# Kernel optimization log

Measured on AMD Instinct MI355X. Metric: run time of the kernel, lower is better.

The kernel has to match this reference:

```python
import jax, jax.numpy as jnp
import numpy as np
import math

B, S, L, D, H, F = 4, 1024, 4, 256, 8, 1024
NUM_LETTERS = 22
VOCAB = NUM_LETTERS + 3
HD = D // H
DISSONANCE = 0.5


def setup_inputs() -> dict:
    key = jax.random.key(0)
    ks = iter(jax.random.split(key, 64))
    r = lambda shape, s=0.05: jax.random.normal(next(ks), shape, dtype=jnp.float32) * s
    inp = {
        'input_roots': jax.random.randint(next(ks), (B, S, 3), 0, VOCAB),
        'gematria': jax.random.uniform(next(ks), (B, S), dtype=jnp.float32),
        'letter_embed': r((VOCAB, D), 0.02),
        'root_proj_w': r((3 * D, D)), 'root_proj_b': jnp.zeros((D,)),
        'root_ln_g': jnp.ones((D,)), 'root_ln_b': jnp.zeros((D,)),
        'input_proj_w': r((2 * D, D)), 'input_proj_b': jnp.zeros((D,)),
        'input_ln_g': jnp.ones((D,)), 'input_ln_b': jnp.zeros((D,)),
        'qw': r((L, D, D)), 'qb': jnp.zeros((L, D)),
        'kw': r((L, D, D)), 'kb': jnp.zeros((L, D)),
        'vw': r((L, D, D)), 'vb': jnp.zeros((L, D)),
        'ow': r((L, D, D)), 'ob': jnp.zeros((L, D)),
        'dist_scale': r((L, H), 0.1), 'diss_sens': jnp.full((L, H), 0.5),
        'ff1w': r((L, D, F)), 'ff1b': jnp.zeros((L, F)),
        'ff2w': r((L, F, D)), 'ff2b': jnp.zeros((L, D)),
        'ln1g': jnp.ones((L, D)), 'ln1b': jnp.zeros((L, D)),
        'ln2g': jnp.ones((L, D)), 'ln2b': jnp.zeros((L, D)),
        'out_ln_g': jnp.ones((D,)), 'out_ln_b': jnp.zeros((D,)),
        'h1w': r((D, NUM_LETTERS)), 'h1b': jnp.zeros((NUM_LETTERS,)),
        'h2w': r((D, NUM_LETTERS)), 'h2b': jnp.zeros((NUM_LETTERS,)),
        'h3w': r((D, NUM_LETTERS)), 'h3b': jnp.zeros((NUM_LETTERS,)),
    }
    return inp


def _ln(x, g, b):
    m = jnp.mean(x, -1, keepdims=True)
    v = jnp.mean(jnp.square(x - m), -1, keepdims=True)
    return (x - m) * jax.lax.rsqrt(v + 1e-5) * g + b


def _rtl_pos(s, d):
    # flipped sinusoidal PE: token j gets original position s-1-j
    pos = (s - 1 - jnp.arange(s, dtype=jnp.float32))[:, None]
    div = jnp.exp(jnp.arange(0, d, 2, dtype=jnp.float32) * (-(math.log(10000.0) / d)))
    pe = jnp.zeros((s, d))
    pe = pe.at[:, 0::2].set(jnp.sin(pos * div))
    pe = pe.at[:, 1::2].set(jnp.cos(pos * div))
    return pe


def _forward(input_roots, gematria, letter_embed, root_proj_w, root_proj_b,
             root_ln_g, root_ln_b, input_proj_w, input_proj_b, input_ln_g, input_ln_b,
             qw, qb, kw, kb, vw, vb, ow, ob, dist_scale, diss_sens,
             ff1w, ff1b, ff2w, ff2b, ln1g, ln1b, ln2g, ln2b,
             out_ln_g, out_ln_b, h1w, h1b, h2w, h2b, h3w, h3b):
    b, s, _ = input_roots.shape
    # root encoder
    letters = letter_embed[input_roots]                      # (b,s,3,D)
    root_emb = _ln(letters.reshape(b, s, 3 * D) @ root_proj_w + root_proj_b, root_ln_g, root_ln_b)
    # gematria sinusoidal
    angles = (gematria[..., None] * 500.0) * jnp.exp(
        jnp.arange(0, D, 2, dtype=jnp.float32) * (-(math.log(10000.0) / D)))
    gem_emb = jnp.concatenate([jnp.sin(angles), jnp.cos(angles)], axis=-1)  # (b,s,D)
    x = jnp.concatenate([root_emb, gem_emb], axis=-1) @ input_proj_w + input_proj_b
    x = _ln(x + _rtl_pos(s, D)[None], input_ln_g, input_ln_b)
    # distance matrix |i-j| shared across layers
    pos = jnp.arange(s, dtype=jnp.float32)
    dist = jnp.abs(pos[None, :] - pos[:, None])              # (s,s)
    scale = 1.0 / math.sqrt(HD)
    for i in range(L):
        normed = _ln(x, ln1g[i], ln1b[i])
        Q = (normed @ qw[i] + qb[i]).reshape(b, s, H, HD)
        K = (normed @ kw[i] + kb[i]).reshape(b, s, H, HD)
        V = (normed @ vw[i] + vb[i]).reshape(b, s, H, HD)
        scores = jnp.einsum('bqhd,bkhd->bhqk', Q, K) * scale
        penalty = dist_scale[i] * (1.0 - DISSONANCE * diss_sens[i])  # (H,)
        bias = -jnp.abs(penalty)[:, None, None] * dist[None]         # (H,s,s)
        attn = jax.nn.softmax(scores + bias[None], axis=-1)
        out = jnp.einsum('bhqk,bkhd->bqhd', attn, V).reshape(b, s, D)
        x = x + (out @ ow[i] + ob[i])
        h = _ln(x, ln2g[i], ln2b[i])
        x = x + (jax.nn.gelu(h @ ff1w[i] + ff1b[i], approximate=False) @ ff2w[i] + ff2b[i])
    x = _ln(x, out_ln_g, out_ln_b)
    return (x @ h1w + h1b, x @ h2w + h2b, x @ h3w + h3b)


def reference(input_roots, gematria, letter_embed, root_proj_w, root_proj_b,
              root_ln_g, root_ln_b, input_proj_w, input_proj_b, input_ln_g, input_ln_b,
              qw, qb, kw, kb, vw, vb, ow, ob, dist_scale, diss_sens,
              ff1w, ff1b, ff2w, ff2b, ln1g, ln1b, ln2g, ln2b,
              out_ln_g, out_ln_b, h1w, h1b, h2w, h2b, h3w, h3b):
    return _forward(input_roots, gematria, letter_embed, root_proj_w, root_proj_b,
                    root_ln_g, root_ln_b, input_proj_w, input_proj_b, input_ln_g, input_ln_b,
                    qw, qb, kw, kb, vw, vb, ow, ob, dist_scale, diss_sens,
                    ff1w, ff1b, ff2w, ff2b, ln1g, ln1b, ln2g, ln2b,
                    out_ln_g, out_ln_b, h1w, h1b, h2w, h2b, h3w, h3b)
```

## Files before the change

### kernel.cpp

```cpp
#include <hip/hip_runtime.h>
#include <hip/hip_bf16.h>
#include <math.h>

#define NTOK   4096
#define SEQ    1024
#define DMODEL 256
#define NHEAD  8
#define FDIM   1024
#define NLAYER 4

typedef __attribute__((ext_vector_type(8))) short short8v;
typedef __attribute__((ext_vector_type(4))) float f32x4;

#define LDS3(p) ((__attribute__((address_space(3))) unsigned int*)(p))
#define GAS1(p) ((const __attribute__((address_space(1))) unsigned int*)(p))

__device__ __forceinline__ void gl_lds16(const void* g, void* l) {
    __builtin_amdgcn_global_load_lds(GAS1(g), LDS3(l), 16, 0, 0);
}
__device__ __forceinline__ short f2bf(float v) {
    __hip_bfloat16 h = __float2bfloat16(v);
    return __builtin_bit_cast(short, h);
}

__device__ __forceinline__ void blockSum2(float& s1, float& s2, float* red) {
    #pragma unroll
    for (int off = 32; off > 0; off >>= 1) {
        s1 += __shfl_down(s1, off);
        s2 += __shfl_down(s2, off);
    }
    int lane = threadIdx.x & 63, w = threadIdx.x >> 6;
    __syncthreads();
    if (lane == 0) { red[w] = s1; red[4 + w] = s2; }
    __syncthreads();
    s1 = red[0] + red[1] + red[2] + red[3];
    s2 = red[4] + red[5] + red[6] + red[7];
}

struct TD { const float* src; __hip_bfloat16* dst; int K; int M; };
struct TDs { TD d[29]; };

__global__ __launch_bounds__(256) void transpose_kernel(TDs p) {
    __shared__ float ld[32][33];
    TD d = p.d[blockIdx.y];
    int tm = (d.M + 31) >> 5;
    int kt = blockIdx.x / tm, mt = blockIdx.x % tm;
    if (kt * 32 >= d.K) return;
    int tx = threadIdx.x & 31, ty = threadIdx.x >> 5;
    #pragma unroll
    for (int r = 0; r < 4; ++r) {
        int k = kt * 32 + ty + r * 8, m = mt * 32 + tx;
        if (m < d.M) ld[ty + r * 8][tx] = d.src[(long)k * d.M + m];
    }
    __syncthreads();
    #pragma unroll
    for (int r = 0; r < 4; ++r) {
        int m = mt * 32 + ty + r * 8, k = kt * 32 + tx;
        if (m < d.M) d.dst[(long)m * d.K + k] = __float2bfloat16(ld[tx][ty + r * 8]);
    }
}

template <int TM, int TN, int EPI>
__global__ __launch_bounds__(256) void mm_kernel(
    const __hip_bfloat16* __restrict__ A, const __hip_bfloat16* __restrict__ Bw,
    const float* __restrict__ bias, float* __restrict__ Cf,
    __hip_bfloat16* __restrict__ Cb, int N, int K, int M,
    const float* __restrict__ b2, const float* __restrict__ b3,
    __hip_bfloat16* __restrict__ Ck, __hip_bfloat16* __restrict__ Cv)
{
    constexpr int BK = 64;
    __shared__ __align__(16) short As[TM * BK];
    __shared__ __align__(16) short Bs[TN * BK];
    const int tid = threadIdx.x;
    const int lane = tid & 63, wid = tid >> 6;
    const int wr = wid >> 1, wc = wid & 1;
    const int n0 = blockIdx.y * TM, m0 = blockIdx.x * TN;
    const int l15 = lane & 15, g = lane >> 4;
    constexpr int FM = (TM / 32 > 0) ? TM / 32 : 1;
    constexpr int FN = TN / 32;
    f32x4 acc[FM][FN] = {};

    for (int k0 = 0; k0 < K; k0 += BK) {
        constexpr int CA = TM * 8;
        __syncthreads();
        #pragma unroll
        for (int j = 0; j < (CA + 255) / 256; ++j) {
            int cid = tid + j * 256;
            if (CA % 256 == 0 || cid < CA) {
                int r = cid >> 3, sl = cid & 7, ss = sl ^ (r & 7);
                gl_lds16(A + (long)(n0 + r) * K + k0 + ss * 8, (char*)As + cid * 16);
            }
        }
        constexpr int CB = TN * 8;
        #pragma unroll
        for (int j = 0; j < CB / 256; ++j) {
            int cid = tid + j * 256;
            int r = cid >> 3, sl = cid & 7, ss = sl ^ (r & 7);
            gl_lds16(Bw + (long)(m0 + r) * K + k0 + ss * 8, (char*)Bs + cid * 16);
        }
        __syncthreads();
        #pragma unroll
        for (int ks = 0; ks < 2; ++ks) {
            short8v af[FM], bfr[FN];
            #pragma unroll
            for (int mi = 0; mi < FM; ++mi) {
                int row = wr * (TM / 2) + mi * 16 + l15;
                int slot = (ks * 4 + g) ^ (row & 7);
                af[mi] = *(const short8v*)((const char*)As + row * (BK * 2) + slot * 16);
            }
            #pragma unroll
            for (int ni = 0; ni < FN; ++ni) {
                int row = wc * (TN / 2) + ni * 16 + l15;
                int slot = (ks * 4 + g) ^ (row & 7);
                bfr[ni] = *(const short8v*)((const char*)Bs + row * (BK * 2) + slot * 16);
            }
            #pragma unroll
            for (int mi = 0; mi < FM; ++mi)
                #pragma unroll
                for (int ni = 0; ni < FN; ++ni)
                    acc[mi][ni] = __builtin_amdgcn_mfma_f32_16x16x32_bf16(
                        af[mi], bfr[ni], acc[mi][ni], 0, 0, 0);
        }
    }

    #pragma unroll
    for (int mi = 0; mi < FM; ++mi) {
        #pragma unroll
        for (int ni = 0; ni < FN; ++ni) {
            int colb = m0 + wc * (TN / 2) + ni * 16 + l15;
            float bv;
            if (EPI == 6) bv = (colb < 256) ? bias[colb] : (colb < 512) ? b2[colb - 256] : b3[colb - 512];
            else bv = bias[colb];
            if (EPI == 6 && colb >= 512) {
                int c2 = colb - 512;
                int h = c2 >> 5, dd = c2 & 31;
                int row0 = n0 + wr * (TM / 2) + mi * 16 + g * 4;
                int bb = row0 >> 10, ss = row0 & 1023;
                short4 pk;
                pk.x = f2bf(acc[mi][ni][0] + bv);
                pk.y = f2bf(acc[mi][ni][1] + bv);
                pk.z = f2bf(acc[mi][ni][2] + bv);
                pk.w = f2bf(acc[mi][ni][3] + bv);
                *(short4*)((short*)Cv + ((long)((bb * 8 + h) * 32 + dd) << 10) + ss) = pk;
            } else {
                #pragma unroll
                for (int i = 0; i < 4; ++i) {
                    int row = n0 + wr * (TM / 2) + mi * 16 + g * 4 + i;
                    float v = acc[mi][ni][i] + bv;
                    if (EPI == 0) Cf[(long)row * M + colb] = v;
                    else if (EPI == 2) {
                        v = 0.5f * v * (1.f + erff(v * 0.70710678f));
                        Cb[(long)row * M + colb] = __float2bfloat16(v);
                    } else if (EPI == 5) {
                        if (colb < 66) {
                            int hd = colb / 22, jj = colb - hd * 22;
                            Cf[(long)hd * (NTOK * 22) + (long)row * 22 + jj] = v;
                        }
                    } else if (EPI == 6) {
                        __hip_bfloat16* dst = (colb < 256) ? Cb : Ck;
                        int cc = (colb < 256) ? colb : colb - 256;
                        dst[(long)row * 256 + cc] = __float2bfloat16(v);
                    }
                }
            }
        }
    }
}

__global__ __launch_bounds__(256) void mm_wide_ln_kernel(
    const __hip_bfloat16* __restrict__ A, const __hip_bfloat16* __restrict__ Bw,
    const float* __restrict__ bias, float* __restrict__ xio,
    __hip_bfloat16* __restrict__ nrm, const float* __restrict__ lng,
    const float* __restrict__ lnb, int K)
{
    constexpr int BK = 64;
    __shared__ __align__(16) short As[16 * BK];
    __shared__ __align__(16) short Bs[256 * BK];
    __shared__ float2 red2[4][16];
    const int tid = threadIdx.x;
    const int lane = tid & 63, wid = tid >> 6;
    const int l15 = lane & 15, g = lane >> 4;
    const int n0 = blockIdx.x * 16;
    f32x4 acc[4] = {};

    for (int k0 = 0; k0 < K; k0 += BK) {
        __syncthreads();
        if (tid < 128) {
            int r = tid >> 3, sl = tid & 7, ss = sl ^ (r & 7);
            gl_lds16(A + (long)(n0 + r) * K + k0 + ss * 8, (char*)As + tid * 16);
        }
        #pragma unroll
        for (int j = 0; j < 8; ++j) {
            int cid = tid + j * 256;
            int r = cid >> 3, sl = cid & 7, ss = sl ^ (r & 7);
            gl_lds16(Bw + (long)r * K + k0 + ss * 8, (char*)Bs + cid * 16);
        }
        __syncthreads();
        #pragma unroll
        for (int ks = 0; ks < 2; ++ks) {
            short8v af;
            {
                int slot = (ks * 4 + g) ^ (l15 & 7);
                af = *(const short8v*)((const char*)As + l15 * (BK * 2) + slot * 16);
            }
            #pragma unroll
            for (int ni = 0; ni < 4; ++ni) {
                int brow = wid * 64 + ni * 16 + l15;
                int slot = (ks * 4 + g) ^ (brow & 7);
                short8v bfr = *(const short8v*)((const char*)Bs + brow * (BK * 2) + slot * 16);
                acc[ni] = __builtin_amdgcn_mfma_f32_16x16x32_bf16(af, bfr, acc[ni], 0, 0, 0);
            }
        }
    }

    float pvt[4][4];
    float rs[4] = {0.f, 0.f, 0.f, 0.f}, rq[4] = {0.f, 0.f, 0.f, 0.f};
    #pragma unroll
    for (int ni = 0; ni < 4; ++ni) {
        int col = wid * 64 + ni * 16 + l15;
        float bv = bias[col];
        #pragma unroll
        for (int i = 0; i < 4; ++i) {
            int row = n0 + g * 4 + i;
            float v = acc[ni][i] + bv + xio[(long)row * 256 + col];
            pvt[ni][i] = v;
            rs[i] += v;
            rq[i] += v * v;
        }
    }
    #pragma unroll
    for (int i = 0; i < 4; ++i) {
        #pragma unroll
        for (int off = 8; off; off >>= 1) {
            rs[i] += __shfl_xor(rs[i], off);
            rq[i] += __shfl_xor(rq[i], off);
        }
    }
    __syncthreads();
    if (l15 == 0) {
        #pragma unroll
        for (int i = 0; i < 4; ++i)
            red2[wid][g * 4 + i] = make_float2(rs[i], rq[i]);
    }
    __syncthreads();
    #pragma unroll
    for (int i = 0; i < 4; ++i) {
        int lr = g * 4 + i;
        float s1 = red2[0][lr].x + red2[1][lr].x + red2[2][lr].x + red2[3][lr].x;
        float s2 = red2[0][lr].y + red2[1][lr].y + red2[2][lr].y + red2[3][lr].y;
        float mean = s1 * (1.f / 256.f);
        float var = s2 * (1.f / 256.f) - mean * mean;
        float rsx = rsqrtf(var + 1e-5f);
        int row = n0 + lr;
        #pragma unroll
        for (int ni = 0; ni < 4; ++ni) {
            int col = wid * 64 + ni * 16 + l15;
            float v = pvt[ni][i];
            xio[(long)row * 256 + col] = v;
            nrm[(long)row * 256 + col] =
                __float2bfloat16((v - mean) * rsx * lng[col] + lnb[col]);
        }
    }
}

__global__ __launch_bounds__(256) void attn_mfma_kernel(
    const __hip_bfloat16* __restrict__ Q, const __hip_bfloat16* __restrict__ Kx,
    const __hip_bfloat16* __restrict__ Vt, __hip_bfloat16* __restrict__ Oa,
    const float* __restrict__ dsc, const float* __restrict__ dss)
{
    __shared__ __align__(16) short Qs[64 * 32];
    __shared__ __align__(16) short Ks[64 * 32];
    __shared__ __align__(16) short Vs[32 * 64];
    __shared__ __align__(16) short Ps[4 * 16 * 64];
    const int tid = threadIdx.x, lane = tid & 63, wid = tid >> 6;
    const int qt = blockIdx.x, bh = blockIdx.y, b = bh >> 3, h = bh & 7;
    const float pen = fabsf(dsc[h] * (1.f - 0.5f * dss[h]));
    const int l15 = lane & 15, g = lane >> 4;
    const float scale = 0.17677669529663689f;

    {
        int r = tid >> 2, sl = tid & 3, ss = sl ^ (r & 3);
        gl_lds16(Q + ((long)(b * SEQ + qt * 64 + r) * DMODEL + h * 32) + ss * 8,
                 (char*)Qs + tid * 16);
    }
    float mrow[4], lrow[4];
    #pragma unroll
    for (int i = 0; i < 4; ++i) { mrow[i] = -1e30f; lrow[i] = 0.f; }
    f32x4 oacc[2] = {};
    float qpos[4];
    #pragma unroll
    for (int i = 0; i < 4; ++i) qpos[i] = (float)(qt * 64 + wid * 16 + g * 4 + i);

    for (int kt = 0; kt < 16; ++kt) {
        {
            int r = tid >> 2, sl = tid & 3, ss = sl ^ (r & 3);
            gl_lds16(Kx + ((long)(b * SEQ + kt * 64 + r) * DMODEL + h * 32) + ss * 8,
                     (char*)Ks + tid * 16);
            int d = tid >> 3, sl8 = tid & 7, ss8 = sl8 ^ (d & 7);
            gl_lds16(Vt + ((long)(bh * 32 + d) << 10) + kt * 64 + ss8 * 8,
                     (char*)Vs + tid * 16);
        }
        __syncthreads();

        short8v aq;
        {
            int row = wid * 16 + l15;
            int slot = g ^ (row & 3);
            aq = *(const short8v*)((const char*)Qs + row * 64 + slot * 16);
        }
        f32x4 sa[4];
        #pragma unroll
        for (int ni = 0; ni < 4; ++ni) {
            int krow = ni * 16 + l15;
            int slot = g ^ (krow & 3);
            short8v bk = *(const short8v*)((const char*)Ks + krow * 64 + slot * 16);
            f32x4 z = {0.f, 0.f, 0.f, 0.f};
            sa[ni] = __builtin_amdgcn_mfma_f32_16x16x32_bf16(aq, bk, z, 0, 0, 0);
        }
        float sc[4][4], tmax[4];
        #pragma unroll
        for (int i = 0; i < 4; ++i) tmax[i] = -1e30f;
        #pragma unroll
        for (int ni = 0; ni < 4; ++ni) {
            float kpos = (float)(kt * 64 + ni * 16 + l15);
            #pragma unroll
            for (int i = 0; i < 4; ++i) {
                float v = sa[ni][i] * scale - pen * fabsf(qpos[i] - kpos);
                sc[ni][i] = v;
                tmax[i] = fmaxf(tmax[i], v);
            }
        }
        #pragma unroll
        for (int i = 0; i < 4; ++i) {
            #pragma unroll
            for (int off = 8; off; off >>= 1)
                tmax[i] = fmaxf(tmax[i], __shfl_xor(tmax[i], off));
        }
        float fac[4];
        #pragma unroll
        for (int i = 0; i < 4; ++i) {
            float mn = fmaxf(mrow[i], tmax[i]);
            fac[i] = __expf(mrow[i] - mn);
            mrow[i] = mn;
        }
        float ps[4] = {0.f, 0.f, 0.f, 0.f};
        #pragma unroll
        for (int ni = 0; ni < 4; ++ni) {
            #pragma unroll
            for (int i = 0; i < 4; ++i) {
                float p = __expf(sc[ni][i] - mrow[i]);
                ps[i] += p;
                int lr = g * 4 + i, key = ni * 16 + l15;
                int slot = (key >> 3) ^ (lr & 7);
                *(short*)((char*)Ps + wid * 2048 + lr * 128 + slot * 16 + (key & 7) * 2) = f2bf(p);
            }
        }
        #pragma unroll
        for (int i = 0; i < 4; ++i) {
            #pragma unroll
            for (int off = 8; off; off >>= 1) ps[i] += __shfl_xor(ps[i], off);
            lrow[i] = lrow[i] * fac[i] + ps[i];
        }
        #pragma unroll
        for (int n2 = 0; n2 < 2; ++n2)
            #pragma unroll
            for (int i = 0; i < 4; ++i) oacc[n2][i] *= fac[i];

        #pragma unroll
        for (int ks = 0; ks < 2; ++ks) {
            int lr = l15;
            int slot = (ks * 4 + g) ^ (lr & 7);
            short8v pa = *(const short8v*)((const char*)Ps + wid * 2048 + lr * 128 + slot * 16);
            #pragma unroll
            for (int n2 = 0; n2 < 2; ++n2) {
                int d = n2 * 16 + l15;
                int vslot = (ks * 4 + g) ^ (d & 7);
                short8v vb = *(const short8v*)((const char*)Vs + d * 128 + vslot * 16);
                oacc[n2] = __builtin_amdgcn_mfma_f32_16x16x32_bf16(pa, vb, oacc[n2], 0, 0, 0);
            }
        }
        __syncthreads();
    }
    #pragma unroll
    for (int n2 = 0; n2 < 2; ++n2) {
        #pragma unroll
        for (int i = 0; i < 4; ++i) {
            float v = oacc[n2][i] / lrow[i];
            long row = b * SEQ + qt * 64 + wid * 16 + g * 4 + i;
            Oa[row * DMODEL + h * 32 + n2 * 16 + l15] = __float2bfloat16(v);
        }
    }
}

__global__ __launch_bounds__(256) void gather_kernel(
    const int* __restrict__ roots, const float* __restrict__ letE,
    __hip_bfloat16* __restrict__ cat,
    const float* __restrict__ h1b, const float* __restrict__ h2b,
    const float* __restrict__ h3b, float* __restrict__ biascat)
{
    const int n = blockIdx.x, t = threadIdx.x;
    int r0 = roots[n * 3 + 0], r1 = roots[n * 3 + 1], r2 = roots[n * 3 + 2];
    cat[(long)n * 768 + t]       = __float2bfloat16(letE[r0 * DMODEL + t]);
    cat[(long)n * 768 + 256 + t] = __float2bfloat16(letE[r1 * DMODEL + t]);
    cat[(long)n * 768 + 512 + t] = __float2bfloat16(letE[r2 * DMODEL + t]);
    if (n == 0 && t < 66)
        biascat[t] = (t < 22) ? h1b[t] : (t < 44) ? h2b[t - 22] : h3b[t - 44];
}

__global__ __launch_bounds__(256) void ln_gem_kernel(
    const float* __restrict__ tmpf, const float* __restrict__ gem,
    const float* __restrict__ gg, const float* __restrict__ gb,
    __hip_bfloat16* __restrict__ catin)
{
    __shared__ float red[8];
    const int n = blockIdx.x, t = threadIdx.x;
    const float LC = 0.0359778921f;
    float v = tmpf[(long)n * DMODEL + t];
    float s1 = v, s2 = v * v;
    blockSum2(s1, s2, red);
    float mean = s1 * (1.f / 256.f);
    float var = s2 * (1.f / 256.f) - mean * mean;
    catin[(long)n * 512 + t] =
        __float2bfloat16((v - mean) * rsqrtf(var + 1e-5f) * gg[t] + gb[t]);
    float gv = gem[n];
    int j = (t < 128) ? t : t - 128;
    float ang = gv * 500.f * expf(-(float)(2 * j) * LC);
    catin[(long)n * 512 + 256 + t] = __float2bfloat16((t < 128) ? sinf(ang) : cosf(ang));
}

__global__ __launch_bounds__(256) void ln_pe2_kernel(
    const float* __restrict__ tmpf, const float* __restrict__ gg,
    const float* __restrict__ gb, const float* __restrict__ g1,
    const float* __restrict__ b1, float* __restrict__ x,
    __hip_bfloat16* __restrict__ nrm)
{
    __shared__ float red[8];
    const int n = blockIdx.x, t = threadIdx.x;
    const int s = n & (SEQ - 1);
    const float LC = 0.0359778921f;
    float pos = (float)(SEQ - 1 - s);
    float dv = expf(-(float)(t & ~1) * LC);
    float pe = (t & 1) ? cosf(pos * dv) : sinf(pos * dv);
    float v = tmpf[(long)n * DMODEL + t] + pe;
    float s1 = v, s2 = v * v;
    blockSum2(s1, s2, red);
    float mean = s1 * (1.f / 256.f);
    float var = s2 * (1.f / 256.f) - mean * mean;
    float xv = (v - mean) * rsqrtf(var + 1e-5f) * gg[t] + gb[t];
    x[(long)n * DMODEL + t] = xv;
    s1 = xv; s2 = xv * xv;
    blockSum2(s1, s2, red);
    mean = s1 * (1.f / 256.f);
    var = s2 * (1.f / 256.f) - mean * mean;
    nrm[(long)n * DMODEL + t] =
        __float2bfloat16((xv - mean) * rsqrtf(var + 1e-5f) * g1[t] + b1[t]);
}

extern "C" void kernel_launch(void* const* d_in, const int* in_sizes, int n_in,
                              void* d_out, int out_size, void* d_ws, size_t ws_size,
                              hipStream_t stream)
{
    const int*   roots = (const int*)  d_in[0];
    const float* gem   = (const float*)d_in[1];
    const float* letE  = (const float*)d_in[2];
    const float* rpw   = (const float*)d_in[3];
    const float* rpb   = (const float*)d_in[4];
    const float* rlg   = (const float*)d_in[5];
    const float* rlb   = (const float*)d_in[6];
    const float* ipw   = (const float*)d_in[7];
    const float* ipb   = (const float*)d_in[8];
    const float* ilg   = (const float*)d_in[9];
    const float* ilb   = (const float*)d_in[10];
    const float* qw    = (const float*)d_in[11];
    const float* qb    = (const float*)d_in[12];
    const float* kw    = (const float*)d_in[13];
    const float* kb    = (const float*)d_in[14];
    const float* vw    = (const float*)d_in[15];
    const float* vb    = (const float*)d_in[16];
    const float* ow    = (const float*)d_in[17];
    const float* ob    = (const float*)d_in[18];
    const float* dsc   = (const float*)d_in[19];
    const float* dss   = (const float*)d_in[20];
    const float* ff1w  = (const float*)d_in[21];
    const float* ff1b  = (const float*)d_in[22];
    const float* ff2w  = (const float*)d_in[23];
    const float* ff2b  = (const float*)d_in[24];
    const float* ln1g  = (const float*)d_in[25];
    const float* ln1b  = (const float*)d_in[26];
    const float* ln2g  = (const float*)d_in[27];
    const float* ln2b  = (const float*)d_in[28];
    const float* olng  = (const float*)d_in[29];
    const float* olnb  = (const float*)d_in[30];
    const float* h1w   = (const float*)d_in[31];
    const float* h1b   = (const float*)d_in[32];
    const float* h2w   = (const float*)d_in[33];
    const float* h2b   = (const float*)d_in[34];
    const float* h3w   = (const float*)d_in[35];
    const float* h3b   = (const float*)d_in[36];

    char* wsb = (char*)d_ws;
    float*          x    = (float*)         (wsb + (0l  << 20));
    float*          tmpf = (float*)         (wsb + (4l  << 20));
    __hip_bfloat16* nrm  = (__hip_bfloat16*)(wsb + (8l  << 20));
    __hip_bfloat16* qbuf = (__hip_bfloat16*)(wsb + (10l << 20));
    __hip_bfloat16* kbuf = (__hip_bfloat16*)(wsb + (12l << 20));
    __hip_bfloat16* vtb  = (__hip_bfloat16*)(wsb + (14l << 20));
    __hip_bfloat16* aob  = (__hip_bfloat16*)(wsb + (16l << 20));
    __hip_bfloat16* hbb  = (__hip_bfloat16*)(wsb + (18l << 20));
    __hip_bfloat16* catb  = hbb;
    __hip_bfloat16* catin = qbuf;
    __hip_bfloat16* wb   = (__hip_bfloat16*)(wsb + (26l << 20));
    float*          biascat = (float*)      (wsb + (34l << 20));

    __hip_bfloat16* rpw_t  = wb;
    __hip_bfloat16* ipw_t  = wb + 196608;
    __hip_bfloat16* qkv_t  = wb + 327680;
    __hip_bfloat16* ow_t   = wb + 1114112;
    __hip_bfloat16* ff1w_t = wb + 1376256;
    __hip_bfloat16* ff2w_t = wb + 2424832;
    __hip_bfloat16* head_t = wb + 3473408;

    hipMemsetAsync(head_t, 0, 32768 * 2, stream);

    TDs td;
    td.d[0] = {rpw, rpw_t, 768, 256};
    td.d[1] = {ipw, ipw_t, 512, 256};
    for (int l = 0; l < 4; ++l) {
        td.d[2 + l]  = {qw + l * 65536,  qkv_t + l * 196608 + 0,      256, 256};
        td.d[6 + l]  = {kw + l * 65536,  qkv_t + l * 196608 + 65536,  256, 256};
        td.d[10 + l] = {vw + l * 65536,  qkv_t + l * 196608 + 131072, 256, 256};
        td.d[14 + l] = {ow + l * 65536,  ow_t + l * 65536,  256, 256};
        td.d[18 + l] = {ff1w + l * 262144, ff1w_t + l * 262144, 256, 1024};
        td.d[22 + l] = {ff2w + l * 262144, ff2w_t + l * 262144, 1024, 256};
    }
    td.d[26] = {h1w, head_t + 0 * 22 * 256, 256, 22};
    td.d[27] = {h2w, head_t + 1 * 22 * 256, 256, 22};
    td.d[28] = {h3w, head_t + 2 * 22 * 256, 256, 22};
    transpose_kernel<<<dim3(256, 29), 256, 0, stream>>>(td);

    gather_kernel<<<NTOK, 256, 0, stream>>>(roots, letE, catb, h1b, h2b, h3b, biascat);
    mm_kernel<32, 64, 0><<<dim3(4, 128), 256, 0, stream>>>(
        catb, rpw_t, rpb, tmpf, nullptr, NTOK, 768, 256, nullptr, nullptr, nullptr, nullptr);
    ln_gem_kernel<<<NTOK, 256, 0, stream>>>(tmpf, gem, rlg, rlb, catin);
    mm_kernel<32, 64, 0><<<dim3(4, 128), 256, 0, stream>>>(
        catin, ipw_t, ipb, tmpf, nullptr, NTOK, 512, 256, nullptr, nullptr, nullptr, nullptr);
    ln_pe2_kernel<<<NTOK, 256, 0, stream>>>(tmpf, ilg, ilb, ln1g, ln1b, x, nrm);

    for (int l = 0; l < NLAYER; ++l) {
        mm_kernel<64, 64, 6><<<dim3(12, 64), 256, 0, stream>>>(
            nrm, qkv_t + l * 196608, qb + l * 256, nullptr, qbuf, NTOK, 256, 768,
            kb + l * 256, vb + l * 256, kbuf, vtb);
        attn_mfma_kernel<<<dim3(16, 32), 256, 0, stream>>>(qbuf, kbuf, vtb, aob,
                                                           dsc + l * 8, dss + l * 8);
        mm_wide_ln_kernel<<<dim3(NTOK / 16), 256, 0, stream>>>(
            aob, ow_t + l * 65536, ob + l * 256, x, nrm,
            ln2g + l * 256, ln2b + l * 256, 256);
        mm_kernel<64, 64, 2><<<dim3(16, 64), 256, 0, stream>>>(
            nrm, ff1w_t + l * 262144, ff1b + l * 1024, nullptr, hbb, NTOK, 256, 1024,
            nullptr, nullptr, nullptr, nullptr);
        const float* ng = (l == 3) ? olng : ln1g + (l + 1) * 256;
        const float* nb = (l == 3) ? olnb : ln1b + (l + 1) * 256;
        mm_wide_ln_kernel<<<dim3(NTOK / 16), 256, 0, stream>>>(
            hbb, ff2w_t + l * 262144, ff2b + l * 256, x, nrm, ng, nb, 1024);
    }
    mm_kernel<32, 64, 5><<<dim3(2, 128), 256, 0, stream>>>(
        nrm, head_t, biascat, (float*)d_out, nullptr, NTOK, 256, 128,
        nullptr, nullptr, nullptr, nullptr);
}
```

Before: 472.2 us.

## Double-buffer LDS tiles in GEMMs and attention; transpose score MFMA

Adds ping-pong LDS buffers to the generic GEMM, the wide GEMM+LayerNorm kernel and the flash-attention kernel. The next K-tile (or K/V tile) is issued with async global-to-LDS loads while MFMAs run on the current one, which removes one barrier per iteration and hides load latency. Attention now computes S^T = K·Q so each lane owns one query row. That makes the softmax max/sum reductions a two-step cross-lane shuffle and lets P be written as packed short4 stores, with the Q fragment hoisted out of the loop. This doubles LDS use per block, which may lower occupancy.

Result: faster. 435.0 us (-7.9%).

```diff
diff --git a/kernel.cpp b/kernel.cpp
--- a/kernel.cpp
+++ b/kernel.cpp
@@ -69,8 +69,8 @@
     __hip_bfloat16* __restrict__ Ck, __hip_bfloat16* __restrict__ Cv)
 {
     constexpr int BK = 64;
-    __shared__ __align__(16) short As[TM * BK];
-    __shared__ __align__(16) short Bs[TN * BK];
+    __shared__ __align__(16) short As[2][TM * BK];
+    __shared__ __align__(16) short Bs[2][TN * BK];
     const int tid = threadIdx.x;
     const int lane = tid & 63, wid = tid >> 6;
     const int wr = wid >> 1, wc = wid & 1;
@@ -79,16 +79,16 @@
     constexpr int FM = (TM / 32 > 0) ? TM / 32 : 1;
     constexpr int FN = TN / 32;
     f32x4 acc[FM][FN] = {};
-
-    for (int k0 = 0; k0 < K; k0 += BK) {
+    const int nt = K >> 6;
+
+    auto stage = [&](int buf, int k0) {
         constexpr int CA = TM * 8;
-        __syncthreads();
         #pragma unroll
         for (int j = 0; j < (CA + 255) / 256; ++j) {
             int cid = tid + j * 256;
             if (CA % 256 == 0 || cid < CA) {
                 int r = cid >> 3, sl = cid & 7, ss = sl ^ (r & 7);
-                gl_lds16(A + (long)(n0 + r) * K + k0 + ss * 8, (char*)As + cid * 16);
+                gl_lds16(A + (long)(n0 + r) * K + k0 + ss * 8, (char*)As[buf] + cid * 16);
             }
         }
         constexpr int CB = TN * 8;
@@ -96,9 +96,15 @@
         for (int j = 0; j < CB / 256; ++j) {
             int cid = tid + j * 256;
             int r = cid >> 3, sl = cid & 7, ss = sl ^ (r & 7);
-            gl_lds16(Bw + (long)(m0 + r) * K + k0 + ss * 8, (char*)Bs + cid * 16);
-        }
-        __syncthreads();
+            gl_lds16(Bw + (long)(m0 + r) * K + k0 + ss * 8, (char*)Bs[buf] + cid * 16);
+        }
+    };
+
+    stage(0, 0);
+    __syncthreads();
+    for (int t = 0; t < nt; ++t) {
+        int cur = t & 1;
+        if (t + 1 < nt) stage(cur ^ 1, (t + 1) * BK);
         #pragma unroll
         for (int ks = 0; ks < 2; ++ks) {
             short8v af[FM], bfr[FN];
@@ -106,13 +112,13 @@
             for (int mi = 0; mi < FM; ++mi) {
                 int row = wr * (TM / 2) + mi * 16 + l15;
                 int slot = (ks * 4 + g) ^ (row & 7);
-                af[mi] = *(const short8v*)((const char*)As + row * (BK * 2) + slot * 16);
+                af[mi] = *(const short8v*)((const char*)As[cur] + row * (BK * 2) + slot * 16);
             }
             #pragma unroll
             for (int ni = 0; ni < FN; ++ni) {
                 int row = wc * (TN / 2) + ni * 16 + l15;
                 int slot = (ks * 4 + g) ^ (row & 7);
-                bfr[ni] = *(const short8v*)((const char*)Bs + row * (BK * 2) + slot * 16);
+                bfr[ni] = *(const short8v*)((const char*)Bs[cur] + row * (BK * 2) + slot * 16);
             }
             #pragma unroll
             for (int mi = 0; mi < FM; ++mi)
@@ -121,6 +127,7 @@
                     acc[mi][ni] = __builtin_amdgcn_mfma_f32_16x16x32_bf16(
                         af[mi], bfr[ni], acc[mi][ni], 0, 0, 0);
         }
+        __syncthreads();
     }
 
     #pragma unroll
@@ -174,43 +181,50 @@
     const float* __restrict__ lnb, int K)
 {
     constexpr int BK = 64;
-    __shared__ __align__(16) short As[16 * BK];
-    __shared__ __align__(16) short Bs[256 * BK];
+    __shared__ __align__(16) short As[2][16 * BK];
+    __shared__ __align__(16) short Bs[2][256 * BK];
     __shared__ float2 red2[4][16];
     const int tid = threadIdx.x;
     const int lane = tid & 63, wid = tid >> 6;
     const int l15 = lane & 15, g = lane >> 4;
     const int n0 = blockIdx.x * 16;
     f32x4 acc[4] = {};
-
-    for (int k0 = 0; k0 < K; k0 += BK) {
-        __syncthreads();
+    const int nt = K >> 6;
+
+    auto stage = [&](int buf, int k0) {
         if (tid < 128) {
             int r = tid >> 3, sl = tid & 7, ss = sl ^ (r & 7);
-            gl_lds16(A + (long)(n0 + r) * K + k0 + ss * 8, (char*)As + tid * 16);
+            gl_lds16(A + (long)(n0 + r) * K + k0 + ss * 8, (char*)As[buf] + tid * 16);
         }
         #pragma unroll
         for (int j = 0; j < 8; ++j) {
             int cid = tid + j * 256;
             int r = cid >> 3, sl = cid & 7, ss = sl ^ (r & 7);
-            gl_lds16(Bw + (long)r * K + k0 + ss * 8, (char*)Bs + cid * 16);
-        }
-        __syncthreads();
+            gl_lds16(Bw + (long)r * K + k0 + ss * 8, (char*)Bs[buf] + cid * 16);
+        }
+    };
+
+    stage(0, 0);
+    __syncthreads();
+    for (int t = 0; t < nt; ++t) {
+        int cur = t & 1;
+        if (t + 1 < nt) stage(cur ^ 1, (t + 1) * BK);
         #pragma unroll
         for (int ks = 0; ks < 2; ++ks) {
             short8v af;
             {
                 int slot = (ks * 4 + g) ^ (l15 & 7);
-                af = *(const short8v*)((const char*)As + l15 * (BK * 2) + slot * 16);
+                af = *(const short8v*)((const char*)As[cur] + l15 * (BK * 2) + slot * 16);
             }
             #pragma unroll
             for (int ni = 0; ni < 4; ++ni) {
                 int brow = wid * 64 + ni * 16 + l15;
                 int slot = (ks * 4 + g) ^ (brow & 7);
-                short8v bfr = *(const short8v*)((const char*)Bs + brow * (BK * 2) + slot * 16);
+                short8v bfr = *(const short8v*)((const char*)Bs[cur] + brow * (BK * 2) + slot * 16);
                 acc[ni] = __builtin_amdgcn_mfma_f32_16x16x32_bf16(af, bfr, acc[ni], 0, 0, 0);
             }
         }
+        __syncthreads();
     }
 
     float pvt[4][4];
@@ -269,8 +283,8 @@
     const float* __restrict__ dsc, const float* __restrict__ dss)
 {
     __shared__ __align__(16) short Qs[64 * 32];
-    __shared__ __align__(16) short Ks[64 * 32];
-    __shared__ __align__(16) short Vs[32 * 64];
+    __shared__ __align__(16) short Ks[2][64 * 32];
+    __shared__ __align__(16) short Vs[2][32 * 64];
     __shared__ __align__(16) short Ps[4 * 16 * 64];
     const int tid = threadIdx.x, lane = tid & 63, wid = tid >> 6;
     const int qt = blockIdx.x, bh = blockIdx.y, b = bh >> 3, h = bh & 7;
@@ -278,114 +292,108 @@
     const int l15 = lane & 15, g = lane >> 4;
     const float scale = 0.17677669529663689f;
 
+    auto stageKV = [&](int buf, int kt) {
+        int r = tid >> 2, sl = tid & 3, ss = sl ^ (r & 3);
+        gl_lds16(Kx + ((long)(b * SEQ + kt * 64 + r) * DMODEL + h * 32) + ss * 8,
+                 (char*)Ks[buf] + tid * 16);
+        int d = tid >> 3, sl8 = tid & 7, ss8 = sl8 ^ (d & 7);
+        gl_lds16(Vt + ((long)(bh * 32 + d) << 10) + kt * 64 + ss8 * 8,
+                 (char*)Vs[buf] + tid * 16);
+    };
+
     {
         int r = tid >> 2, sl = tid & 3, ss = sl ^ (r & 3);
         gl_lds16(Q + ((long)(b * SEQ + qt * 64 + r) * DMODEL + h * 32) + ss * 8,
                  (char*)Qs + tid * 16);
     }
-    float mrow[4], lrow[4];
-    #pragma unroll
-    for (int i = 0; i < 4; ++i) { mrow[i] = -1e30f; lrow[i] = 0.f; }
+    stageKV(0, 0);
+    __syncthreads();
+
+    short8v bq;
+    {
+        int row = wid * 16 + l15;
+        int slot = g ^ (row & 3);
+        bq = *(const short8v*)((const char*)Qs + row * 64 + slot * 16);
+    }
+
+    float m = -1e30f, l = 0.f;
     f32x4 oacc[2] = {};
-    float qpos[4];
-    #pragma unroll
-    for (int i = 0; i < 4; ++i) qpos[i] = (float)(qt * 64 + wid * 16 + g * 4 + i);
+    const float qpos = (float)(qt * 64 + wid * 16 + l15);
+    char* pbase = (char*)Ps + wid * 2048 + l15 * 128;
 
     for (int kt = 0; kt < 16; ++kt) {
-        {
-            int r = tid >> 2, sl = tid & 3, ss = sl ^ (r & 3);
-            gl_lds16(Kx + ((long)(b * SEQ + kt * 64 + r) * DMODEL + h * 32) + ss * 8,
-                     (char*)Ks + tid * 16);
-            int d = tid >> 3, sl8 = tid & 7, ss8 = sl8 ^ (d & 7);
-            gl_lds16(Vt + ((long)(bh * 32 + d) << 10) + kt * 64 + ss8 * 8,
-                     (char*)Vs + tid * 16);
-        }
-        __syncthreads();
-
-        short8v aq;
-        {
-            int row = wid * 16 + l15;
-            int slot = g ^ (row & 3);
-            aq = *(const short8v*)((const char*)Qs + row * 64 + slot * 16);
-        }
-        f32x4 sa[4];
+        int cur = kt & 1;
+        if (kt < 15) stageKV(cur ^ 1, kt + 1);
+
+        float s[4][4];
+        float smax = -1e30f;
         #pragma unroll
         for (int ni = 0; ni < 4; ++ni) {
             int krow = ni * 16 + l15;
             int slot = g ^ (krow & 3);
-            short8v bk = *(const short8v*)((const char*)Ks + krow * 64 + slot * 16);
+            short8v ak = *(const short8v*)((const char*)Ks[cur] + krow * 64 + slot * 16);
             f32x4 z = {0.f, 0.f, 0.f, 0.f};
-            sa[ni] = __builtin_amdgcn_mfma_f32_16x16x32_bf16(aq, bk, z, 0, 0, 0);
-        }
-        float sc[4][4], tmax[4];
-        #pragma unroll
-        for (int i = 0; i < 4; ++i) tmax[i] = -1e30f;
+            f32x4 sa = __builtin_amdgcn_mfma_f32_16x16x32_bf16(ak, bq, z, 0, 0, 0);
+            float kbase = (float)(kt * 64 + ni * 16 + g * 4);
+            #pragma unroll
+            for (int i = 0; i < 4; ++i) {
+                float v = sa[i] * scale - pen * fabsf(qpos - (kbase + (float)i));
+                s[ni][i] = v;
+                smax = fmaxf(smax, v);
+            }
+        }
+        smax = fmaxf(smax, __shfl_xor(smax, 16));
+        smax = fmaxf(smax, __shfl_xor(smax, 32));
+        float mn = fmaxf(m, smax);
+        float fac = __expf(m - mn);
+        m = mn;
+        float ps = 0.f;
         #pragma unroll
         for (int ni = 0; ni < 4; ++ni) {
-            float kpos = (float)(kt * 64 + ni * 16 + l15);
+            short4 pk;
             #pragma unroll
             for (int i = 0; i < 4; ++i) {
-                float v = sa[ni][i] * scale - pen * fabsf(qpos[i] - kpos);
-                sc[ni][i] = v;
-                tmax[i] = fmaxf(tmax[i], v);
-            }
-        }
-        #pragma unroll
-        for (int i = 0; i < 4; ++i) {
-            #pragma unroll
-            for (int off = 8; off; off >>= 1)
-                tmax[i] = fmaxf(tmax[i], __shfl_xor(tmax[i], off));
-        }
-        float fac[4];
-        #pragma unroll
-        for (int i = 0; i < 4; ++i) {
-            float mn = fmaxf(mrow[i], tmax[i]);
-            fac[i] = __expf(mrow[i] - mn);
-            mrow[i] = mn;
-        }
-        float ps[4] = {0.f, 0.f, 0.f, 0.f};
-        #pragma unroll
-        for (int ni = 0; ni < 4; ++ni) {
-            #pragma unroll
-            for (int i = 0; i < 4; ++i) {
-                float p = __expf(sc[ni][i] - mrow[i]);
-                ps[i] += p;
-                int lr = g * 4 + i, key = ni * 16 + l15;
-                int slot = (key >> 3) ^ (lr & 7);
-                *(short*)((char*)Ps + wid * 2048 + lr * 128 + slot * 16 + (key & 7) * 2) = f2bf(p);
-            }
-        }
-        #pragma unroll
-        for (int i = 0; i < 4; ++i) {
-            #pragma unroll
-            for (int off = 8; off; off >>= 1) ps[i] += __shfl_xor(ps[i], off);
-            lrow[i] = lrow[i] * fac[i] + ps[i];
-        }
+                float p = __expf(s[ni][i] - mn);
+                ps += p;
+                ((short*)&pk)[i] = f2bf(p);
+            }
+            int slot = (ni * 2 + (g >> 1)) ^ (l15 & 7);
+            *(short4*)(pbase + slot * 16 + (g & 1) * 8) = pk;
+        }
+        ps += __shfl_xor(ps, 16);
+        ps += __shfl_xor(ps, 32);
+        l = l * fac + ps;
+
+        float facr[4];
+        #pragma unroll
+        for (int i = 0; i < 4; ++i) facr[i] = __shfl(fac, g * 4 + i);
         #pragma unroll
         for (int n2 = 0; n2 < 2; ++n2)
             #pragma unroll
-            for (int i = 0; i < 4; ++i) oacc[n2][i] *= fac[i];
+            for (int i = 0; i < 4; ++i) oacc[n2][i] *= facr[i];
 
         #pragma unroll
         for (int ks = 0; ks < 2; ++ks) {
-            int lr = l15;
-            int slot = (ks * 4 + g) ^ (lr & 7);
-            short8v pa = *(const short8v*)((const char*)Ps + wid * 2048 + lr * 128 + slot * 16);
+            int slot = (ks * 4 + g) ^ (l15 & 7);
+            short8v pa = *(const short8v*)(pbase + slot * 16);
             #pragma unroll
             for (int n2 = 0; n2 < 2; ++n2) {
                 int d = n2 * 16 + l15;
                 int vslot = (ks * 4 + g) ^ (d & 7);
-                short8v vb = *(const short8v*)((const char*)Vs + d * 128 + vslot * 16);
+                short8v vb = *(const short8v*)((const char*)Vs[cur] + d * 128 + vslot * 16);
                 oacc[n2] = __builtin_amdgcn_mfma_f32_16x16x32_bf16(pa, vb, oacc[n2], 0, 0, 0);
             }
         }
         __syncthreads();
     }
+    float lr[4];
+    #pragma unroll
+    for (int i = 0; i < 4; ++i) lr[i] = __shfl(l, g * 4 + i);
     #pragma unroll
     for (int n2 = 0; n2 < 2; ++n2) {
         #pragma unroll
         for (int i = 0; i < 4; ++i) {
-            float v = oacc[n2][i] / lrow[i];
+            float v = oacc[n2][i] / lr[i];
             long row = b * SEQ + qt * 64 + wid * 16 + g * 4 + i;
             Oa[row * DMODEL + h * 32 + n2 * 16 + l15] = __float2bfloat16(v);
         }
```
